# Kernel optimization log

Hardware: AMD Instinct MI355X
Metric: run time of the kernel (lower is better)

The kernel has to match this reference:

```python
import jax, jax.numpy as jnp
import numpy as np

B, S, D, F, E, K = 2, 2048, 1024, 4096, 8, 2


def setup_inputs() -> dict:
    key = jax.random.key(0)
    ks = jax.random.split(key, 6)
    s = 0.02  # init scale
    return {
        "x": jax.random.normal(ks[0], (B, S, D), dtype=jnp.float32),
        "Wr": jax.random.normal(ks[1], (D, E), dtype=jnp.float32) * s,
        "br": jnp.zeros((E,), dtype=jnp.float32),
        "W1": jax.random.normal(ks[2], (E, D, F), dtype=jnp.float32) * s,
        "b1": jnp.zeros((E, F), dtype=jnp.float32),
        "W2": jax.random.normal(ks[3], (E, F, D), dtype=jnp.float32) * s,
        "b2": jnp.zeros((E, D), dtype=jnp.float32),
        "top_k": K,
    }


def reference(x, Wr, br, W1, b1, W2, b2, top_k):
    b, s, d = x.shape
    e = Wr.shape[1]
    xt = x.reshape(-1, d)                              # [T, D], T = b*s
    logits = xt @ Wr + br                              # [T, E]
    probs = jax.nn.softmax(logits, axis=-1)            # [T, E] router probabilities
    topw, topi = jax.lax.top_k(probs, top_k)           # [T, K] each
    # combine weight per (token, expert): weight if expert in token's top-k else 0
    cw = jnp.sum(jax.nn.one_hot(topi, e, dtype=x.dtype) * topw[..., None], axis=1)  # [T, E]
    # dense grouped FFN: every expert over every token, then weighted combine
    h = jax.nn.relu(jnp.einsum('td,edf->tef', xt, W1) + b1)   # [T, E, F]
    y = jnp.einsum('tef,efd->ted', h, W2) + b2                # [T, E, D]
    out = jnp.einsum('te,ted->td', cw, y).reshape(b, s, d)    # [B, S, D]
    return out, probs.reshape(b, s, e)
```

## Files before the change

### kernel.cpp

```cpp
#include <hip/hip_runtime.h>
#include <hip/hip_bf16.h>


#define T_TOK 4096
#define D_DIM 1024
#define F_DIM 4096
#define E_NUM 8
#define CAP_ROWS 10240
#define N_TILES (CAP_ROWS/256)

typedef __attribute__((ext_vector_type(8))) short short8v;
typedef __attribute__((ext_vector_type(8))) unsigned short ushort8v;
typedef __attribute__((ext_vector_type(4))) float f32x4;

static __device__ __forceinline__ unsigned short f2bf(float f){
  union { float f; unsigned u; } v; v.f = f;
  unsigned r = (v.u + 0x7fffu + ((v.u >> 16) & 1u)) >> 16;
  return (unsigned short)r;
}
static __device__ __forceinline__ float bf2f(unsigned short s){
  union { unsigned u; float f; } v; v.u = ((unsigned)s) << 16;
  return v.f;
}

static __device__ __forceinline__ void gload16(const void* g, void* l) {
  __builtin_amdgcn_global_load_lds(
      (const __attribute__((address_space(1))) unsigned int*)g,
      (__attribute__((address_space(3))) unsigned int*)l, 16, 0, 0);
}

__global__ __launch_bounds__(256) void k_init(int* counts, int* cursor,
                                              int* rows_token, float* rows_w){
  const int gid = blockIdx.x * 256 + threadIdx.x;
  if (gid < E_NUM) counts[gid] = 0;
  else if (gid < 2*E_NUM) cursor[gid - E_NUM] = 0;
  if (gid < CAP_ROWS) { rows_token[gid] = 0; rows_w[gid] = 0.f; }
}

__global__ __launch_bounds__(256) void k_router(
    const float* __restrict__ x, const float* __restrict__ Wr,
    const float* __restrict__ br, float* __restrict__ probs_out,
    int* __restrict__ topi, float* __restrict__ topw, int* __restrict__ counts,
    unsigned short* __restrict__ xbf)
{
  const int lane = threadIdx.x & 63;
  const int t = blockIdx.x * 4 + (threadIdx.x >> 6);
  float xv[16];
  #pragma unroll
  for (int i = 0; i < 16; ++i) xv[i] = x[(size_t)t*D_DIM + i*64 + lane];
  #pragma unroll
  for (int i = 0; i < 16; ++i) xbf[(size_t)t*D_DIM + i*64 + lane] = f2bf(xv[i]);
  float pe[E_NUM];
  #pragma unroll
  for (int e = 0; e < E_NUM; ++e) {
    float p = 0.f;
    #pragma unroll
    for (int i = 0; i < 16; ++i) p += xv[i] * Wr[(i*64 + lane)*E_NUM + e];
    #pragma unroll
    for (int off = 32; off >= 1; off >>= 1) p += __shfl_xor(p, off);
    pe[e] = p + br[e];
  }
  float m = pe[0];
  #pragma unroll
  for (int e = 1; e < E_NUM; ++e) m = fmaxf(m, pe[e]);
  float s = 0.f;
  #pragma unroll
  for (int e = 0; e < E_NUM; ++e) { pe[e] = expf(pe[e] - m); s += pe[e]; }
  const float inv = 1.f / s;
  int e1 = 0; float v1 = pe[0];
  #pragma unroll
  for (int e = 1; e < E_NUM; ++e) if (pe[e] > v1) { v1 = pe[e]; e1 = e; }
  int e2 = (e1 == 0) ? 1 : 0; float v2 = pe[e2];
  #pragma unroll
  for (int e = 0; e < E_NUM; ++e) if (e != e1 && pe[e] > v2) { v2 = pe[e]; e2 = e; }
  if (lane == 0) {
    #pragma unroll
    for (int e = 0; e < E_NUM; ++e) probs_out[(size_t)t*E_NUM + e] = pe[e] * inv;
    topi[t*2+0] = e1; topw[t*2+0] = v1 * inv;
    topi[t*2+1] = e2; topw[t*2+1] = v2 * inv;
    atomicAdd(&counts[e1], 1);
    atomicAdd(&counts[e2], 1);
  }
}

__global__ __launch_bounds__(256) void k_scan(
    const int* __restrict__ counts, int* __restrict__ pbase,
    int* __restrict__ tile_e)
{
  __shared__ int base_s[E_NUM + 1];
  const int tid = threadIdx.x;
  if (tid == 0) {
    int base = 0;
    #pragma unroll
    for (int e = 0; e < E_NUM; ++e) {
      base_s[e] = base;
      base += ((counts[e] + 255) >> 8) << 8;
    }
    base_s[E_NUM] = base;
  }
  __syncthreads();
  if (tid <= E_NUM) pbase[tid] = base_s[tid];
  if (tid < N_TILES) {
    const int r0 = tid << 8;
    int e = -1;
    #pragma unroll
    for (int k = 0; k < E_NUM; ++k)
      if (r0 >= base_s[k] && r0 < base_s[k+1]) e = k;
    tile_e[tid] = e;
  }
}

__global__ __launch_bounds__(256) void k_assign(
    const int* __restrict__ topi, const float* __restrict__ topw,
    const int* __restrict__ pbase, int* __restrict__ cursor,
    int* __restrict__ rows_token, float* __restrict__ rows_w,
    int* __restrict__ pair_of)
{
  const int t = blockIdx.x * 256 + threadIdx.x;
  if (t < T_TOK) {
    #pragma unroll
    for (int k = 0; k < 2; ++k) {
      const int e = topi[t*2+k];
      const int slot = atomicAdd(&cursor[e], 1);
      const int pid = pbase[e] + slot;
      rows_token[pid] = t;
      rows_w[pid] = topw[t*2+k];
      pair_of[t*2+k] = pid;
    }
  }
}

template<int R, int C>
__global__ __launch_bounds__(256) void k_tcvt(const float* __restrict__ in,
                                              unsigned short* __restrict__ out)
{
  const size_t eo = (size_t)blockIdx.z * R * C;
  const int r0 = blockIdx.y * 64, c0 = blockIdx.x * 64;
  __shared__ unsigned short ls[64][66];
  const int t = threadIdx.x;
  const int rr = t >> 4, cc = (t & 15) * 4;
  #pragma unroll
  for (int p = 0; p < 4; ++p) {
    const float4 v = *(const float4*)&in[eo + (size_t)(r0 + p*16 + rr)*C + c0 + cc];
    ls[p*16+rr][cc+0]=f2bf(v.x); ls[p*16+rr][cc+1]=f2bf(v.y);
    ls[p*16+rr][cc+2]=f2bf(v.z); ls[p*16+rr][cc+3]=f2bf(v.w);
  }
  __syncthreads();
  const int kc = (t & 7) * 8, nn0 = t >> 3;
  #pragma unroll
  for (int p = 0; p < 2; ++p) {
    const int nn = nn0 + p*32;
    ushort8v o;
    #pragma unroll
    for (int j = 0; j < 8; ++j) o[j] = ls[kc + j][nn];
    *(ushort8v*)&out[eo + (size_t)(c0 + nn)*R + r0 + kc] = o;
  }
}

template<bool GATHER, int NDIM, int KFULL, int EPI>
__global__ __launch_bounds__(512, 2) void k_gemm(
    const unsigned short* __restrict__ A,
    const unsigned short* __restrict__ Bt,
    const float* __restrict__ bias,
    const int* __restrict__ tile_e,
    const int* __restrict__ rows_token,
    const float* __restrict__ rows_w,
    unsigned short* __restrict__ outp,
    int nkt, int kch)
{
  const int tot = gridDim.x * gridDim.y;
  int flat = blockIdx.x * gridDim.y + blockIdx.y;
  flat = (flat & 7) * (tot >> 3) + (flat >> 3);
  const int bx = flat / gridDim.y;
  const int by = flat % gridDim.y;
  const int e = tile_e[by];
  if (e < 0) return;
  const int rt = by * 256;
  const int ntc = bx * 256;
  const int koff = blockIdx.z * kch;
  __shared__ __align__(16) unsigned short LB[2][512 * 64];
  const int tid = threadIdx.x;
  const int lane = tid & 63;
  const int w = tid >> 6;
  const int lr = lane >> 3;
  const int g  = (lane & 7) ^ lr;
  const unsigned short* gp[8];
  unsigned lbase[8];
  if (w < 4) {
    #pragma unroll
    for (int i = 0; i < 8; ++i) {
      const int rl = w*64 + i*8 + lr;
      const int rowidx = GATHER ? rows_token[rt + rl] : (rt + rl);
      gp[i] = A + (size_t)rowidx * KFULL + koff + g*8;
      lbase[i] = (unsigned)((w*64 + i*8) * 64);
    }
  } else {
    const unsigned short* Be = Bt + (size_t)e * NDIM * KFULL;
    #pragma unroll
    for (int i = 0; i < 8; ++i) {
      const int rl = (w-4)*64 + i*8 + lr;
      gp[i] = Be + (size_t)(ntc + rl) * KFULL + koff + g*8;
      lbase[i] = (unsigned)((256 + (w-4)*64 + i*8) * 64);
    }
  }
  const int wr = w >> 2, wc = w & 3;
  const int cl = lane & 15, rgb = lane >> 4;
  const int sz = cl & 7;
  f32x4 acc[8][4] = {};

  #define STG4(tt, bb, c0)                                    \
    { const int _ko = (tt) * 64;                              \
      gload16(gp[c0+0] + _ko, &LB[bb][lbase[c0+0]]);          \
      gload16(gp[c0+1] + _ko, &LB[bb][lbase[c0+1]]);          \
      gload16(gp[c0+2] + _ko, &LB[bb][lbase[c0+2]]);          \
      gload16(gp[c0+3] + _ko, &LB[bb][lbase[c0+3]]); }
  #define LGK0  asm volatile("s_waitcnt lgkmcnt(0)" ::: "memory")
  #define BAR   __builtin_amdgcn_s_barrier()

  STG4(0, 0, 0) STG4(0, 0, 4)
  STG4(1, 1, 0)
  asm volatile("s_waitcnt vmcnt(4)" ::: "memory");
  BAR;

  for (int t = 0; t < nkt; ++t) {
    const int bb = t & 1;
    const unsigned short* Sb = &LB[bb][0];
    short8v a[4][2], b[4][2];
    #pragma unroll
    for (int m = 0; m < 4; ++m) {
      a[m][0] = *(const short8v*)&Sb[(wr*128 + m*16 + cl)*64 + ((0*4+rgb)^sz)*8];
      a[m][1] = *(const short8v*)&Sb[(wr*128 + m*16 + cl)*64 + ((1*4+rgb)^sz)*8];
    }
    #pragma unroll
    for (int n = 0; n < 2; ++n) {
      b[n][0] = *(const short8v*)&Sb[(256 + wc*64 + n*16 + cl)*64 + ((0*4+rgb)^sz)*8];
      b[n][1] = *(const short8v*)&Sb[(256 + wc*64 + n*16 + cl)*64 + ((1*4+rgb)^sz)*8];
    }
    if (t + 1 < nkt) STG4(t+1, bb^1, 4)
    BAR; LGK0;
    __builtin_amdgcn_s_setprio(1);
    #pragma unroll
    for (int m = 0; m < 4; ++m)
      #pragma unroll
      for (int n = 0; n < 2; ++n) {
        acc[m][n] = __builtin_amdgcn_mfma_f32_16x16x32_bf16(a[m][0], b[n][0], acc[m][n], 0, 0, 0);
        acc[m][n] = __builtin_amdgcn_mfma_f32_16x16x32_bf16(a[m][1], b[n][1], acc[m][n], 0, 0, 0);
      }
    __builtin_amdgcn_s_setprio(0);
    BAR;
    #pragma unroll
    for (int n = 2; n < 4; ++n) {
      b[n][0] = *(const short8v*)&Sb[(256 + wc*64 + n*16 + cl)*64 + ((0*4+rgb)^sz)*8];
      b[n][1] = *(const short8v*)&Sb[(256 + wc*64 + n*16 + cl)*64 + ((1*4+rgb)^sz)*8];
    }
    BAR; LGK0;
    __builtin_amdgcn_s_setprio(1);
    #pragma unroll
    for (int m = 0; m < 4; ++m)
      #pragma unroll
      for (int n = 2; n < 4; ++n) {
        acc[m][n] = __builtin_amdgcn_mfma_f32_16x16x32_bf16(a[m][0], b[n][0], acc[m][n], 0, 0, 0);
        acc[m][n] = __builtin_amdgcn_mfma_f32_16x16x32_bf16(a[m][1], b[n][1], acc[m][n], 0, 0, 0);
      }
    __builtin_amdgcn_s_setprio(0);
    BAR;
    #pragma unroll
    for (int m = 0; m < 4; ++m) {
      a[m][0] = *(const short8v*)&Sb[(wr*128 + (m+4)*16 + cl)*64 + ((0*4+rgb)^sz)*8];
      a[m][1] = *(const short8v*)&Sb[(wr*128 + (m+4)*16 + cl)*64 + ((1*4+rgb)^sz)*8];
    }
    BAR; LGK0;
    __builtin_amdgcn_s_setprio(1);
    #pragma unroll
    for (int m = 0; m < 4; ++m)
      #pragma unroll
      for (int n = 0; n < 2; ++n) {
        acc[m+4][n] = __builtin_amdgcn_mfma_f32_16x16x32_bf16(a[m][0], b[n][0], acc[m+4][n], 0, 0, 0);
        acc[m+4][n] = __builtin_amdgcn_mfma_f32_16x16x32_bf16(a[m][1], b[n][1], acc[m+4][n], 0, 0, 0);
      }
    __builtin_amdgcn_s_setprio(0);
    BAR;
    if (t + 2 < nkt) {
      STG4(t+2, bb, 0)
      asm volatile("s_waitcnt vmcnt(4)" ::: "memory");
    } else if (t + 1 < nkt) {
      asm volatile("s_waitcnt vmcnt(0)" ::: "memory");
    }
    BAR;
    __builtin_amdgcn_s_setprio(1);
    #pragma unroll
    for (int m = 0; m < 4; ++m)
      #pragma unroll
      for (int n = 2; n < 4; ++n) {
        acc[m+4][n] = __builtin_amdgcn_mfma_f32_16x16x32_bf16(a[m][0], b[n][0], acc[m+4][n], 0, 0, 0);
        acc[m+4][n] = __builtin_amdgcn_mfma_f32_16x16x32_bf16(a[m][1], b[n][1], acc[m+4][n], 0, 0, 0);
      }
    __builtin_amdgcn_s_setprio(0);
    BAR;
  }
  #undef STG4
  #undef LGK0
  #undef BAR

  unsigned short* op = outp;
  if (EPI == 2) op += (size_t)blockIdx.z * CAP_ROWS * NDIM;
  const bool addb = (EPI == 1) || (blockIdx.z == 0);
  const size_t ebias = (size_t)e * NDIM;
  #pragma unroll
  for (int m = 0; m < 8; ++m) {
    const int row = rt + wr*128 + m*16 + rgb*4;
    float4 rw4 = make_float4(0,0,0,0);
    if (EPI == 2) rw4 = *(const float4*)&rows_w[row];
    #pragma unroll
    for (int n = 0; n < 4; ++n) {
      const int col = ntc + wc*64 + n*16 + cl;
      const float bv = addb ? bias[ebias + col] : 0.f;
      #pragma unroll
      for (int r = 0; r < 4; ++r) {
        float v = acc[m][n][r] + bv;
        if (EPI == 1) v = fmaxf(v, 0.f);
        else          v *= ((const float*)&rw4)[r];
        const unsigned short hb = f2bf(v);
        const unsigned short ob = (unsigned short)__shfl_xor((int)(unsigned)hb, 1);
        if ((lane & 1) == 0) {
          const unsigned pk = (unsigned)hb | ((unsigned)ob << 16);
          *(unsigned*)&op[(size_t)(row + r)*NDIM + col] = pk;
        }
      }
    }
  }
}

__global__ __launch_bounds__(256) void k_combine(
    const unsigned short* __restrict__ yp, const int* __restrict__ pair_of,
    float* __restrict__ out, int ksplit)
{
  const int gid = blockIdx.x * 256 + threadIdx.x;
  const int t = gid >> 7;
  const int c = (gid & 127) * 8;
  float o[8] = {0,0,0,0,0,0,0,0};
  #pragma unroll
  for (int k = 0; k < 2; ++k) {
    const int p = pair_of[t*2+k];
    for (int s = 0; s < ksplit; ++s) {
      const ushort8v v = *(const ushort8v*)&yp[((size_t)s*CAP_ROWS + p)*D_DIM + c];
      #pragma unroll
      for (int j = 0; j < 8; ++j) o[j] += bf2f(v[j]);
    }
  }
  float4 o0; o0.x=o[0]; o0.y=o[1]; o0.z=o[2]; o0.w=o[3];
  float4 o1; o1.x=o[4]; o1.y=o[5]; o1.z=o[6]; o1.w=o[7];
  *(float4*)&out[(size_t)t*D_DIM + c]     = o0;
  *(float4*)&out[(size_t)t*D_DIM + c + 4] = o1;
}

extern "C" void kernel_launch(void* const* d_in, const int* in_sizes, int n_in,
                              void* d_out, int out_size, void* d_ws, size_t ws_size,
                              hipStream_t stream)
{
  const float* x  = (const float*)d_in[0];
  const float* Wr = (const float*)d_in[1];
  const float* br = (const float*)d_in[2];
  const float* W1 = (const float*)d_in[3];
  const float* b1 = (const float*)d_in[4];
  const float* W2 = (const float*)d_in[5];
  const float* b2 = (const float*)d_in[6];
  (void)in_sizes; (void)n_in; (void)out_size;

  float* out   = (float*)d_out;
  float* probs = out + (size_t)T_TOK * D_DIM;

  char* w = (char*)d_ws;
  size_t off = 0;
  int*   counts     = (int*)(w + off); off += 256;
  int*   cursor     = (int*)(w + off); off += 256;
  int*   pbase      = (int*)(w + off); off += 512;
  int*   tile_e     = (int*)(w + off); off += 3072;
  int*   topi       = (int*)(w + off); off += (size_t)T_TOK*2*4;
  float* topw       = (float*)(w + off); off += (size_t)T_TOK*2*4;
  int*   pair_of    = (int*)(w + off); off += (size_t)T_TOK*2*4;
  int*   rows_token = (int*)(w + off); off += (size_t)CAP_ROWS*4;
  float* rows_w     = (float*)(w + off); off += (size_t)CAP_ROWS*4;
  off = (off + 255) & ~(size_t)255;
  unsigned short* xbf = (unsigned short*)(w + off); off += (size_t)T_TOK*D_DIM*2;
  unsigned short* Wt  = (unsigned short*)(w + off); off += (size_t)E_NUM*D_DIM*F_DIM*2;
  unsigned short* h   = (unsigned short*)(w + off); off += (size_t)CAP_ROWS*F_DIM*2;
  unsigned short* yp  = (unsigned short*)(w + off);
  const size_t ypart_bytes = (size_t)CAP_ROWS * D_DIM * 2;
  int ksplit = 1;
  if (ws_size >= off + 4 * ypart_bytes) ksplit = 4;
  else if (ws_size >= off + 2 * ypart_bytes) ksplit = 2;
  const int kch2 = F_DIM / ksplit;
  const int nkt2 = kch2 / 64;

  k_init<<<(CAP_ROWS + 255) / 256, 256, 0, stream>>>(counts, cursor, rows_token, rows_w);
  k_router<<<T_TOK / 4, 256, 0, stream>>>(x, Wr, br, probs, topi, topw, counts, xbf);
  k_scan<<<1, 256, 0, stream>>>(counts, pbase, tile_e);
  k_assign<<<T_TOK / 256, 256, 0, stream>>>(topi, topw, pbase, cursor,
                                            rows_token, rows_w, pair_of);
  k_tcvt<D_DIM, F_DIM><<<dim3(F_DIM/64, D_DIM/64, E_NUM), 256, 0, stream>>>(W1, Wt);
  k_gemm<true, F_DIM, D_DIM, 1><<<dim3(F_DIM/256, N_TILES, 1), 512, 0, stream>>>(
      xbf, Wt, b1, tile_e, rows_token, rows_w, h, D_DIM/64, D_DIM);
  k_tcvt<F_DIM, D_DIM><<<dim3(D_DIM/64, F_DIM/64, E_NUM), 256, 0, stream>>>(W2, Wt);
  k_gemm<false, D_DIM, F_DIM, 2><<<dim3(D_DIM/256, N_TILES, ksplit), 512, 0, stream>>>(
      h, Wt, b2, tile_e, rows_token, rows_w, yp, nkt2, kch2);
  k_combine<<<T_TOK * D_DIM / 8 / 256, 256, 0, stream>>>(yp, pair_of, out, ksplit);
}
```

Baseline: 464.2 us.

## Remap GEMM grid to 1D XCD-aware tile order and split B-prefetch stage

```diff
diff --git a/kernel.cpp b/kernel.cpp
--- a/kernel.cpp
+++ b/kernel.cpp
@@ -8,6 +8,7 @@
 #define E_NUM 8
 #define CAP_ROWS 10240
 #define N_TILES (CAP_ROWS/256)
+#define BYG (N_TILES/8)
 
 typedef __attribute__((ext_vector_type(8))) short short8v;
 typedef __attribute__((ext_vector_type(8))) unsigned short ushort8v;
@@ -166,18 +167,20 @@
     const int* __restrict__ rows_token,
     const float* __restrict__ rows_w,
     unsigned short* __restrict__ outp,
-    int nkt, int kch)
-{
-  const int tot = gridDim.x * gridDim.y;
-  int flat = blockIdx.x * gridDim.y + blockIdx.y;
-  flat = (flat & 7) * (tot >> 3) + (flat >> 3);
-  const int bx = flat / gridDim.y;
-  const int by = flat % gridDim.y;
+    int nbx, int nkt, int kch)
+{
+  const int b = blockIdx.x;
+  const int q = b & 7;
+  const int s = b >> 3;
+  const int bxz = s / BYG;
+  const int by  = q * BYG + (s - bxz * BYG);
+  const int bx  = bxz % nbx;
+  const int z   = bxz / nbx;
   const int e = tile_e[by];
   if (e < 0) return;
   const int rt = by * 256;
   const int ntc = bx * 256;
-  const int koff = blockIdx.z * kch;
+  const int koff = z * kch;
   __shared__ __align__(16) unsigned short LB[2][512 * 64];
   const int tid = threadIdx.x;
   const int lane = tid & 63;
@@ -214,6 +217,10 @@
       gload16(gp[c0+1] + _ko, &LB[bb][lbase[c0+1]]);          \
       gload16(gp[c0+2] + _ko, &LB[bb][lbase[c0+2]]);          \
       gload16(gp[c0+3] + _ko, &LB[bb][lbase[c0+3]]); }
+  #define STG2(tt, bb, c0)                                    \
+    { const int _ko = (tt) * 64;                              \
+      gload16(gp[c0+0] + _ko, &LB[bb][lbase[c0+0]]);          \
+      gload16(gp[c0+1] + _ko, &LB[bb][lbase[c0+1]]); }
   #define LGK0  asm volatile("s_waitcnt lgkmcnt(0)" ::: "memory")
   #define BAR   __builtin_amdgcn_s_barrier()
 
@@ -236,7 +243,7 @@
       b[n][0] = *(const short8v*)&Sb[(256 + wc*64 + n*16 + cl)*64 + ((0*4+rgb)^sz)*8];
       b[n][1] = *(const short8v*)&Sb[(256 + wc*64 + n*16 + cl)*64 + ((1*4+rgb)^sz)*8];
     }
-    if (t + 1 < nkt) STG4(t+1, bb^1, 4)
+    if (t + 1 < nkt) STG2(t+1, bb^1, 4)
     BAR; LGK0;
     __builtin_amdgcn_s_setprio(1);
     #pragma unroll
@@ -253,6 +260,7 @@
       b[n][0] = *(const short8v*)&Sb[(256 + wc*64 + n*16 + cl)*64 + ((0*4+rgb)^sz)*8];
       b[n][1] = *(const short8v*)&Sb[(256 + wc*64 + n*16 + cl)*64 + ((1*4+rgb)^sz)*8];
     }
+    if (t + 1 < nkt) STG2(t+1, bb^1, 6)
     BAR; LGK0;
     __builtin_amdgcn_s_setprio(1);
     #pragma unroll
@@ -299,12 +307,13 @@
     BAR;
   }
   #undef STG4
+  #undef STG2
   #undef LGK0
   #undef BAR
 
   unsigned short* op = outp;
-  if (EPI == 2) op += (size_t)blockIdx.z * CAP_ROWS * NDIM;
-  const bool addb = (EPI == 1) || (blockIdx.z == 0);
+  if (EPI == 2) op += (size_t)z * CAP_ROWS * NDIM;
+  const bool addb = (EPI == 1) || (z == 0);
   const size_t ebias = (size_t)e * NDIM;
   #pragma unroll
   for (int m = 0; m < 8; ++m) {
@@ -399,10 +408,10 @@
   k_assign<<<T_TOK / 256, 256, 0, stream>>>(topi, topw, pbase, cursor,
                                             rows_token, rows_w, pair_of);
   k_tcvt<D_DIM, F_DIM><<<dim3(F_DIM/64, D_DIM/64, E_NUM), 256, 0, stream>>>(W1, Wt);
-  k_gemm<true, F_DIM, D_DIM, 1><<<dim3(F_DIM/256, N_TILES, 1), 512, 0, stream>>>(
-      xbf, Wt, b1, tile_e, rows_token, rows_w, h, D_DIM/64, D_DIM);
+  k_gemm<true, F_DIM, D_DIM, 1><<<(F_DIM/256)*N_TILES, 512, 0, stream>>>(
+      xbf, Wt, b1, tile_e, rows_token, rows_w, h, F_DIM/256, D_DIM/64, D_DIM);
   k_tcvt<F_DIM, D_DIM><<<dim3(D_DIM/64, F_DIM/64, E_NUM), 256, 0, stream>>>(W2, Wt);
-  k_gemm<false, D_DIM, F_DIM, 2><<<dim3(D_DIM/256, N_TILES, ksplit), 512, 0, stream>>>(
-      h, Wt, b2, tile_e, rows_token, rows_w, yp, nkt2, kch2);
+  k_gemm<false, D_DIM, F_DIM, 2><<<(D_DIM/256)*N_TILES*ksplit, 512, 0, stream>>>(
+      h, Wt, b2, tile_e, rows_token, rows_w, yp, D_DIM/256, nkt2, kch2);
   k_combine<<<T_TOK * D_DIM / 8 / 256, 256, 0, stream>>>(yp, pair_of, out, ksplit);
 }
```

Result: no change. 461.1 us (-0.7%).
